# Performance work log

Hardware: AMD Instinct MI355X
Metric: run time of the kernel (lower is better)

## Reference

```python
import jax, jax.numpy as jnp
import numpy as np

K = 2            # top-k experts
SCALING = 16.0 / 16.0  # alpha / r


def setup_inputs() -> dict:
    key = jax.random.key(0)
    ks = jax.random.split(key, 7)
    B, T, D, O, E, R = 2, 4096, 2048, 2048, 8, 16
    return {
        "x": jax.random.normal(ks[0], (B, T, D), dtype=jnp.float32),
        "W": jax.random.normal(ks[1], (O, D), dtype=jnp.float32) * (1.0 / np.sqrt(D)),
        "b": jax.random.normal(ks[2], (O,), dtype=jnp.float32) * 0.02,
        "lora_A": jax.random.normal(ks[3], (E, R, D), dtype=jnp.float32) * (1.0 / np.sqrt(D)),
        "lora_B": jax.random.normal(ks[4], (E, O, R), dtype=jnp.float32) * 0.02,
        "gate_w": jax.random.normal(ks[5], (E, D), dtype=jnp.float32) * 0.02,
        "gate_b": jax.random.normal(ks[6], (E,), dtype=jnp.float32) * 0.02,
    }


def reference(x, W, b, lora_A, lora_B, gate_w, gate_b):
    orig_shape = x.shape
    D = orig_shape[-1]
    O = W.shape[0]
    x_flat = x.reshape(-1, D)                                  # [N, D]

    base = x_flat @ W.T + b                                    # [N, O]

    logits = x_flat @ gate_w.T + gate_b                        # [N, E] (eval: no noise)
    topk_logits, topk_idx = jax.lax.top_k(logits, K)           # [N, K]
    gates = jax.nn.softmax(topk_logits, axis=-1)               # [N, K]

    xA = jnp.einsum('nd,erd->ner', x_flat, lora_A)             # [N, E, R]
    delta_all = jnp.einsum('ner,eor->neo', xA, lora_B)         # [N, E, O]

    delta_topk = jnp.take_along_axis(delta_all, topk_idx[:, :, None], axis=1)  # [N, K, O]
    lora_update = jnp.sum(delta_topk * gates[:, :, None], axis=1)              # [N, O]

    out = base + SCALING * lora_update
    return out.reshape(*orig_shape[:-1], O)
```

## Files before the change

### kernel.cpp

```cpp
#include <hip/hip_runtime.h>
#include <hip/hip_bf16.h>
#include <stdint.h>

#define N_ROWS 8192
#define DIM    2048
#define OUTD   2048
#define NEXP   8
#define RNK    16
#define ZCOLS  128
#define KAUG   2176

typedef unsigned short u16;
typedef float  f32x4  __attribute__((ext_vector_type(4)));
typedef __bf16 bf16x8 __attribute__((ext_vector_type(8)));

__device__ __forceinline__ u16 f2bf(float f) {
  unsigned u = __float_as_uint(f);
  return (u16)((u + 0x7fffu + ((u >> 16) & 1u)) >> 16);
}

__global__ __launch_bounds__(256) void k1_convert_gate(
    const float* __restrict__ x, const float* __restrict__ gw,
    const float* __restrict__ gb, u16* __restrict__ xaug,
    int* __restrict__ sel, float* __restrict__ gv)
{
  const int wave = threadIdx.x >> 6;
  const int lane = threadIdx.x & 63;
  const int row0 = blockIdx.x * 8 + wave * 2;

  float xv[2][32];
  #pragma unroll
  for (int rr = 0; rr < 2; ++rr) {
    const float* xr = x + (size_t)(row0 + rr) * DIM;
    #pragma unroll
    for (int i = 0; i < 8; ++i) {
      float4 v = *(const float4*)(xr + (lane * 4 + i * 256));
      xv[rr][i*4+0] = v.x; xv[rr][i*4+1] = v.y;
      xv[rr][i*4+2] = v.z; xv[rr][i*4+3] = v.w;
    }
  }
  #pragma unroll
  for (int rr = 0; rr < 2; ++rr) {
    u16* dst = xaug + (size_t)(row0 + rr) * KAUG;
    #pragma unroll
    for (int i = 0; i < 8; ++i) {
      ushort4 s;
      s.x = f2bf(xv[rr][i*4+0]); s.y = f2bf(xv[rr][i*4+1]);
      s.z = f2bf(xv[rr][i*4+2]); s.w = f2bf(xv[rr][i*4+3]);
      *(ushort4*)(dst + (lane * 4 + i * 256)) = s;
    }
  }
  float lg[2][NEXP];
  #pragma unroll
  for (int e = 0; e < NEXP; ++e) {
    const float* ge = gw + (size_t)e * DIM;
    float s0 = 0.f, s1 = 0.f;
    #pragma unroll
    for (int i = 0; i < 8; ++i) {
      float4 g4 = *(const float4*)(ge + (lane * 4 + i * 256));
      s0 += xv[0][i*4+0]*g4.x + xv[0][i*4+1]*g4.y + xv[0][i*4+2]*g4.z + xv[0][i*4+3]*g4.w;
      s1 += xv[1][i*4+0]*g4.x + xv[1][i*4+1]*g4.y + xv[1][i*4+2]*g4.z + xv[1][i*4+3]*g4.w;
    }
    #pragma unroll
    for (int off = 32; off > 0; off >>= 1) {
      s0 += __shfl_xor(s0, off);
      s1 += __shfl_xor(s1, off);
    }
    lg[0][e] = s0 + gb[e];
    lg[1][e] = s1 + gb[e];
  }
  if (lane == 0) {
    #pragma unroll
    for (int rr = 0; rr < 2; ++rr) {
      int e0 = 0; float m0 = lg[rr][0];
      #pragma unroll
      for (int e = 1; e < NEXP; ++e) if (lg[rr][e] > m0) { m0 = lg[rr][e]; e0 = e; }
      int e1 = (e0 == 0) ? 1 : 0; float m1 = lg[rr][e1];
      #pragma unroll
      for (int e = 0; e < NEXP; ++e) if (e != e0 && lg[rr][e] > m1) { m1 = lg[rr][e]; e1 = e; }
      float t   = expf(m1 - m0);
      float inv = 1.f / (1.f + t);
      int r = row0 + rr;
      sel[2*r] = e0; sel[2*r+1] = e1;
      gv[2*r]  = inv; gv[2*r+1] = t * inv;
    }
  }
}

__global__ __launch_bounds__(256) void k2_weights(
    const float* __restrict__ W, const float* __restrict__ lB,
    const float* __restrict__ lA, u16* __restrict__ waug, u16* __restrict__ ab)
{
  const int t = threadIdx.x;
  const int bid = blockIdx.x;
  if (bid < OUTD) {
    const int o = bid;
    const float* wr = W + (size_t)o * DIM;
    u16* dst = waug + (size_t)o * KAUG;
    #pragma unroll
    for (int i = 0; i < 2; ++i) {
      int c = t * 4 + i * 1024;
      float4 v = *(const float4*)(wr + c);
      ushort4 s; s.x = f2bf(v.x); s.y = f2bf(v.y); s.z = f2bf(v.z); s.w = f2bf(v.w);
      *(ushort4*)(dst + c) = s;
    }
    if (t < ZCOLS) {
      int e = t >> 4, r = t & 15;
      dst[DIM + t] = f2bf(lB[((size_t)e * OUTD + o) * RNK + r]);
    }
  } else {
    const int ar = bid - OUTD;
    const float* src = lA + (size_t)ar * DIM;
    u16* dst = ab + (size_t)ar * DIM;
    #pragma unroll
    for (int i = 0; i < 2; ++i) {
      int c = t * 4 + i * 1024;
      float4 v = *(const float4*)(src + c);
      ushort4 s; s.x = f2bf(v.x); s.y = f2bf(v.y); s.z = f2bf(v.z); s.w = f2bf(v.w);
      *(ushort4*)(dst + c) = s;
    }
  }
}

template <int BM, int BN, int BK, int WM, int WN, int MF, int NF, int EPI>
__global__ __launch_bounds__(WM*WN*64) void gemm_bt(
    const u16* __restrict__ A, int lda,
    const u16* __restrict__ Bm, int ldb,
    int Ksz, int grid_n,
    float* __restrict__ outF, int ldo, const float* __restrict__ bias,
    u16* __restrict__ outZ, int ldz,
    const int* __restrict__ sel, const float* __restrict__ gv)
{
  static_assert(BM == WM * MF * 16 && BN == WN * NF * 16 && BK == 64, "geom");
  constexpr int NW   = WM * WN;
  constexpr int ROWB = BK * 2;
  __shared__ __align__(16) u16 As[2][BM * BK];
  __shared__ __align__(16) u16 Bs[2][BN * BK];

  const int wave = threadIdx.x >> 6;
  const int lane = threadIdx.x & 63;

  int bid = blockIdx.x;
  const int nwg = gridDim.x;
  if ((nwg & 7) == 0) {
    const int cpx = nwg >> 3;
    bid = (bid & 7) * cpx + (bid >> 3);
  }
  const int tm = bid / grid_n;
  const int tn = bid % grid_n;
  const size_t row0 = (size_t)tm * BM;
  const size_t col0 = (size_t)tn * BN;

  auto stage = [&](const u16* __restrict__ g, int ld, size_t r0, int k0,
                   u16* lds, int nrows) {
    const int nch = nrows * (ROWB / 16);
    for (int c0 = wave * 64; c0 < nch; c0 += NW * 64) {
      const int c   = c0 + lane;
      const int r   = c >> 3;
      const int ch  = c & 7;
      const int sch = ch ^ (r & 7);
      const char* src = (const char*)(g + (r0 + (size_t)r) * ld + k0) + (sch << 4);
      __builtin_amdgcn_global_load_lds(
          (__attribute__((address_space(1))) void*)src,
          (__attribute__((address_space(3))) void*)((char*)lds + ((size_t)c0 << 4)),
          16, 0, 0);
    }
  };

  const int wm = wave / WN, wn = wave % WN;
  const int aRow = wm * MF * 16 + (lane & 15);
  const int bRow = wn * NF * 16 + (lane & 15);
  const int kq   = (lane >> 4) << 4;

  f32x4 acc[MF][NF] = {};

  const int nk = Ksz / BK;
  stage(A,  lda, row0, 0, As[0], BM);
  stage(Bm, ldb, col0, 0, Bs[0], BN);
  __syncthreads();

  for (int t = 0; t < nk; ++t) {
    const int cur = t & 1;
    if (t + 1 < nk) {
      stage(A,  lda, row0, (t + 1) * BK, As[cur ^ 1], BM);
      stage(Bm, ldb, col0, (t + 1) * BK, Bs[cur ^ 1], BN);
    }
    const char* ab_ = (const char*)As[cur];
    const char* bb_ = (const char*)Bs[cur];
    #pragma unroll
    for (int ks = 0; ks < BK / 32; ++ks) {
      bf16x8 av[MF], bv[NF];
      #pragma unroll
      for (int mf = 0; mf < MF; ++mf) {
        const int r  = aRow + mf * 16;
        const int bo = (ks * 64 + kq) ^ ((r & 7) << 4);
        av[mf] = *(const bf16x8*)(ab_ + r * ROWB + bo);
      }
      #pragma unroll
      for (int nf = 0; nf < NF; ++nf) {
        const int r  = bRow + nf * 16;
        const int bo = (ks * 64 + kq) ^ ((r & 7) << 4);
        bv[nf] = *(const bf16x8*)(bb_ + r * ROWB + bo);
      }
      #pragma unroll
      for (int mf = 0; mf < MF; ++mf)
        #pragma unroll
        for (int nf = 0; nf < NF; ++nf)
          acc[mf][nf] = __builtin_amdgcn_mfma_f32_16x16x32_bf16(
              av[mf], bv[nf], acc[mf][nf], 0, 0, 0);
    }
    __syncthreads();
  }

  if constexpr (EPI == 1) {
    #pragma unroll
    for (int nf = 0; nf < NF; ++nf) {
      const size_t c = col0 + wn * NF * 16 + nf * 16 + (lane & 15);
      const float bvv = bias[c];
      #pragma unroll
      for (int mf = 0; mf < MF; ++mf) {
        const size_t rb = row0 + wm * MF * 16 + mf * 16 + ((lane >> 4) << 2);
        #pragma unroll
        for (int j = 0; j < 4; ++j)
          outF[(rb + j) * (size_t)ldo + c] = acc[mf][nf][j] + bvv;
      }
    }
  } else {
    #pragma unroll
    for (int mf = 0; mf < MF; ++mf) {
      const size_t rb = row0 + wm * MF * 16 + mf * 16 + ((lane >> 4) << 2);
      #pragma unroll
      for (int j = 0; j < 4; ++j) {
        const size_t rrow = rb + j;
        const int   e0 = sel[2 * rrow],     e1 = sel[2 * rrow + 1];
        const float g0 = gv [2 * rrow],     g1 = gv [2 * rrow + 1];
        #pragma unroll
        for (int nf = 0; nf < NF; ++nf) {
          const int ccol = wn * NF * 16 + nf * 16 + (lane & 15);
          const int e = ccol >> 4;
          const float s = (e == e0) ? g0 : ((e == e1) ? g1 : 0.f);
          outZ[rrow * (size_t)ldz + ccol] = f2bf(acc[mf][nf][j] * s);
        }
      }
    }
  }
}

__global__ __launch_bounds__(512, 2) void gemm256_pipe(
    const u16* __restrict__ A, int lda,
    const u16* __restrict__ Bm, int ldb,
    int Ksz, int grid_n,
    float* __restrict__ outF, int ldo, const float* __restrict__ bias)
{
  __shared__ __align__(16) u16 smem[65536];

  const int tid  = threadIdx.x;
  const int wave = tid >> 6;
  const int lane = tid & 63;

  int bid = blockIdx.x;
  const int nwg = gridDim.x;
  if ((nwg & 7) == 0) {
    const int cpx = nwg >> 3;
    bid = (bid & 7) * cpx + (bid >> 3);
  }
  const int tm = bid / grid_n;
  const int tn = bid % grid_n;
  const size_t row0 = (size_t)tm * 256;
  const size_t col0 = (size_t)tn * 256;

  const int rc  = tid >> 2;
  const int sch = (tid & 3) ^ (rc & 3);
  const char* aS0 = (const char*)(A  + (row0 + (size_t)rc)         * lda) + (sch << 4);
  const char* aS1 = (const char*)(A  + (row0 + (size_t)(rc + 128)) * lda) + (sch << 4);
  const char* bS0 = (const char*)(Bm + (col0 + (size_t)rc)         * ldb) + (sch << 4);
  const char* bS1 = (const char*)(Bm + (col0 + (size_t)(rc + 128)) * ldb) + (sch << 4);
  char* ldsA = (char*)smem + wave * 1024;
  char* ldsB = (char*)smem + 65536 + wave * 1024;

  auto stage = [&](int tt) {
    const size_t ko = (size_t)tt << 6;
    const int    sb = (tt & 3) << 14;
    __builtin_amdgcn_global_load_lds(
        (__attribute__((address_space(1))) void*)(aS0 + ko),
        (__attribute__((address_space(3))) void*)(ldsA + sb), 16, 0, 0);
    __builtin_amdgcn_global_load_lds(
        (__attribute__((address_space(1))) void*)(aS1 + ko),
        (__attribute__((address_space(3))) void*)(ldsA + sb + 8192), 16, 0, 0);
    __builtin_amdgcn_global_load_lds(
        (__attribute__((address_space(1))) void*)(bS0 + ko),
        (__attribute__((address_space(3))) void*)(ldsB + sb), 16, 0, 0);
    __builtin_amdgcn_global_load_lds(
        (__attribute__((address_space(1))) void*)(bS1 + ko),
        (__attribute__((address_space(3))) void*)(ldsB + sb + 8192), 16, 0, 0);
  };

  const int wm = wave >> 2, wn = wave & 3;
  const int swzk = ((lane >> 4) ^ (lane & 3)) << 4;
  const int offA = (wm * 128 + (lane & 15)) * 64 + swzk;
  const int offB = (wn * 64  + (lane & 15)) * 64 + swzk;

  f32x4 acc[8][4] = {};

  const int nk = Ksz / 32;
  stage(0); stage(1); stage(2);

  for (int t = 0; t < nk; ++t) {
    if      (t + 2 < nk) asm volatile("s_waitcnt vmcnt(8)" ::: "memory");
    else if (t + 1 < nk) asm volatile("s_waitcnt vmcnt(4)" ::: "memory");
    else                 asm volatile("s_waitcnt vmcnt(0)" ::: "memory");
    __builtin_amdgcn_s_barrier();
    __builtin_amdgcn_sched_barrier(0);

    if (t + 3 < nk) stage(t + 3);

    const char* sa = (const char*)smem + ((t & 3) << 14);
    const char* sb = (const char*)smem + 65536 + ((t & 3) << 14);

    bf16x8 av[8], bv[4];
    #pragma unroll
    for (int mf = 0; mf < 8; ++mf)
      av[mf] = *(const bf16x8*)(sa + offA + mf * 1024);
    #pragma unroll
    for (int nf = 0; nf < 4; ++nf)
      bv[nf] = *(const bf16x8*)(sb + offB + nf * 1024);

    __builtin_amdgcn_s_setprio(1);
    #pragma unroll
    for (int mf = 0; mf < 8; ++mf)
      #pragma unroll
      for (int nf = 0; nf < 4; ++nf)
        acc[mf][nf] = __builtin_amdgcn_mfma_f32_16x16x32_bf16(
            av[mf], bv[nf], acc[mf][nf], 0, 0, 0);
    __builtin_amdgcn_s_setprio(0);
  }

  #pragma unroll
  for (int nf = 0; nf < 4; ++nf) {
    const size_t c = col0 + wn * 64 + nf * 16 + (lane & 15);
    const float bvv = bias[c];
    #pragma unroll
    for (int mf = 0; mf < 8; ++mf) {
      const size_t rb = row0 + wm * 128 + mf * 16 + ((lane >> 4) << 2);
      #pragma unroll
      for (int j = 0; j < 4; ++j)
        outF[(rb + j) * (size_t)ldo + c] = acc[mf][nf][j] + bvv;
    }
  }
}

extern "C" void kernel_launch(void* const* d_in, const int* in_sizes, int n_in,
                              void* d_out, int out_size, void* d_ws, size_t ws_size,
                              hipStream_t stream) {
  const float* x  = (const float*)d_in[0];
  const float* W  = (const float*)d_in[1];
  const float* b  = (const float*)d_in[2];
  const float* lA = (const float*)d_in[3];
  const float* lB = (const float*)d_in[4];
  const float* gw = (const float*)d_in[5];
  const float* gb = (const float*)d_in[6];
  float* out = (float*)d_out;

  u16*   xaug = (u16*)d_ws;
  u16*   waug = xaug + (size_t)N_ROWS * KAUG;
  u16*   ab   = waug + (size_t)OUTD * KAUG;
  int*   sel  = (int*)(ab + (size_t)ZCOLS * DIM);
  float* gv   = (float*)(sel + 2 * N_ROWS);

  hipLaunchKernelGGL(k1_convert_gate, dim3(N_ROWS / 8), dim3(256), 0, stream,
                     x, gw, gb, xaug, sel, gv);
  hipLaunchKernelGGL(k2_weights, dim3(OUTD + ZCOLS), dim3(256), 0, stream,
                     W, lB, lA, waug, ab);
  hipLaunchKernelGGL((gemm_bt<32, 128, 64, 1, 4, 2, 2, 0>),
                     dim3(N_ROWS / 32), dim3(256), 0, stream,
                     xaug, KAUG, ab, DIM, DIM, 1,
                     (float*)nullptr, 0, (const float*)nullptr,
                     xaug + DIM, KAUG, sel, gv);
  hipLaunchKernelGGL(gemm256_pipe,
                     dim3((N_ROWS / 256) * (OUTD / 256)), dim3(512), 0, stream,
                     xaug, KAUG, waug, KAUG, KAUG, OUTD / 256,
                     out, OUTD, b);
}
```

Baseline: 141.7 us.

## Split-K the LoRA-A GEMM with a separate reduce-gate kernel and use BK=64 main pipeline

The x·A^T GEMM is now a split-K kernel with 128x128 tiles over four K slices. It writes fp32 partials that a new kernel sums, scales by the top-k gate and packs as bf16 into the augmented activation columns. The goal is more parallelism and better tile reuse for the narrow 128-column GEMM. The main 256x256 GEMM moves from a 4-stage BK=32 pipeline to a 2-stage BK=64 one, with two MFMA sub-steps and an extra barrier before the next stage is issued. The cost is an extra kernel launch, fp32 partial traffic through workspace, and less prefetch depth in the main GEMM.

```diff
diff --git a/kernel.cpp b/kernel.cpp
--- a/kernel.cpp
+++ b/kernel.cpp
@@ -9,6 +9,8 @@
 #define RNK    16
 #define ZCOLS  128
 #define KAUG   2176
+#define KSPLIT 4
+#define KSLICE (DIM / KSPLIT)
 
 typedef unsigned short u16;
 typedef float  f32x4  __attribute__((ext_vector_type(4)));
@@ -122,14 +124,11 @@
   }
 }
 
-template <int BM, int BN, int BK, int WM, int WN, int MF, int NF, int EPI>
-__global__ __launch_bounds__(WM*WN*64) void gemm_bt(
+template <int BM, int BN, int BK, int WM, int WN, int MF, int NF>
+__global__ __launch_bounds__(WM*WN*64) void gemm_ksplit(
     const u16* __restrict__ A, int lda,
     const u16* __restrict__ Bm, int ldb,
-    int Ksz, int grid_n,
-    float* __restrict__ outF, int ldo, const float* __restrict__ bias,
-    u16* __restrict__ outZ, int ldz,
-    const int* __restrict__ sel, const float* __restrict__ gv)
+    int Ksz, int gm, float* __restrict__ outP)
 {
   static_assert(BM == WM * MF * 16 && BN == WN * NF * 16 && BK == 64, "geom");
   constexpr int NW   = WM * WN;
@@ -146,10 +145,11 @@
     const int cpx = nwg >> 3;
     bid = (bid & 7) * cpx + (bid >> 3);
   }
-  const int tm = bid / grid_n;
-  const int tn = bid % grid_n;
+  const int tm  = bid % gm;
+  const int ksl = bid / gm;
   const size_t row0 = (size_t)tm * BM;
-  const size_t col0 = (size_t)tn * BN;
+  const u16* Ak = A  + (size_t)ksl * Ksz;
+  const u16* Bk = Bm + (size_t)ksl * Ksz;
 
   auto stage = [&](const u16* __restrict__ g, int ld, size_t r0, int k0,
                    u16* lds, int nrows) {
@@ -175,15 +175,15 @@
   f32x4 acc[MF][NF] = {};
 
   const int nk = Ksz / BK;
-  stage(A,  lda, row0, 0, As[0], BM);
-  stage(Bm, ldb, col0, 0, Bs[0], BN);
+  stage(Ak, lda, row0, 0, As[0], BM);
+  stage(Bk, ldb, 0,    0, Bs[0], BN);
   __syncthreads();
 
   for (int t = 0; t < nk; ++t) {
     const int cur = t & 1;
     if (t + 1 < nk) {
-      stage(A,  lda, row0, (t + 1) * BK, As[cur ^ 1], BM);
-      stage(Bm, ldb, col0, (t + 1) * BK, Bs[cur ^ 1], BN);
+      stage(Ak, lda, row0, (t + 1) * BK, As[cur ^ 1], BM);
+      stage(Bk, ldb, 0,    (t + 1) * BK, Bs[cur ^ 1], BN);
     }
     const char* ab_ = (const char*)As[cur];
     const char* bb_ = (const char*)Bs[cur];
@@ -212,38 +212,42 @@
     __syncthreads();
   }
 
-  if constexpr (EPI == 1) {
-    #pragma unroll
-    for (int nf = 0; nf < NF; ++nf) {
-      const size_t c = col0 + wn * NF * 16 + nf * 16 + (lane & 15);
-      const float bvv = bias[c];
-      #pragma unroll
-      for (int mf = 0; mf < MF; ++mf) {
-        const size_t rb = row0 + wm * MF * 16 + mf * 16 + ((lane >> 4) << 2);
-        #pragma unroll
-        for (int j = 0; j < 4; ++j)
-          outF[(rb + j) * (size_t)ldo + c] = acc[mf][nf][j] + bvv;
-      }
-    }
-  } else {
+  float* op = outP + (size_t)ksl * N_ROWS * ZCOLS;
+  #pragma unroll
+  for (int nf = 0; nf < NF; ++nf) {
+    const int c = wn * NF * 16 + nf * 16 + (lane & 15);
     #pragma unroll
     for (int mf = 0; mf < MF; ++mf) {
       const size_t rb = row0 + wm * MF * 16 + mf * 16 + ((lane >> 4) << 2);
       #pragma unroll
-      for (int j = 0; j < 4; ++j) {
-        const size_t rrow = rb + j;
-        const int   e0 = sel[2 * rrow],     e1 = sel[2 * rrow + 1];
-        const float g0 = gv [2 * rrow],     g1 = gv [2 * rrow + 1];
-        #pragma unroll
-        for (int nf = 0; nf < NF; ++nf) {
-          const int ccol = wn * NF * 16 + nf * 16 + (lane & 15);
-          const int e = ccol >> 4;
-          const float s = (e == e0) ? g0 : ((e == e1) ? g1 : 0.f);
-          outZ[rrow * (size_t)ldz + ccol] = f2bf(acc[mf][nf][j] * s);
-        }
-      }
-    }
-  }
+      for (int j = 0; j < 4; ++j)
+        op[(rb + j) * ZCOLS + c] = acc[mf][nf][j];
+    }
+  }
+}
+
+__global__ __launch_bounds__(256) void k3b_reduce_gate(
+    const float* __restrict__ zpart, const int* __restrict__ sel,
+    const float* __restrict__ gv, u16* __restrict__ xaug)
+{
+  const int idx = blockIdx.x * 256 + threadIdx.x;
+  const int row = idx >> 5;
+  const int c4  = (idx & 31) << 2;
+  const float* zr = zpart + (size_t)row * ZCOLS + c4;
+  const size_t sl = (size_t)N_ROWS * ZCOLS;
+  float4 s = *(const float4*)zr;
+  #pragma unroll
+  for (int k = 1; k < KSPLIT; ++k) {
+    float4 v = *(const float4*)(zr + k * sl);
+    s.x += v.x; s.y += v.y; s.z += v.z; s.w += v.w;
+  }
+  const int e  = c4 >> 4;
+  const int e0 = sel[2 * row], e1 = sel[2 * row + 1];
+  const float g = (e == e0) ? gv[2 * row] : ((e == e1) ? gv[2 * row + 1] : 0.f);
+  ushort4 o;
+  o.x = f2bf(s.x * g); o.y = f2bf(s.y * g);
+  o.z = f2bf(s.z * g); o.w = f2bf(s.w * g);
+  *(ushort4*)(xaug + (size_t)row * KAUG + DIM + c4) = o;
 }
 
 __global__ __launch_bounds__(512, 2) void gemm256_pipe(
@@ -269,62 +273,71 @@
   const size_t row0 = (size_t)tm * 256;
   const size_t col0 = (size_t)tn * 256;
 
-  const int rc  = tid >> 2;
-  const int sch = (tid & 3) ^ (rc & 3);
-  const char* aS0 = (const char*)(A  + (row0 + (size_t)rc)         * lda) + (sch << 4);
-  const char* aS1 = (const char*)(A  + (row0 + (size_t)(rc + 128)) * lda) + (sch << 4);
-  const char* bS0 = (const char*)(Bm + (col0 + (size_t)rc)         * ldb) + (sch << 4);
-  const char* bS1 = (const char*)(Bm + (col0 + (size_t)(rc + 128)) * ldb) + (sch << 4);
+  const int l3  = lane >> 3;
+  const int sch = ((lane & 7) ^ l3) << 4;
+  const char* aSrc = (const char*)(A  + (row0 + (size_t)(wave * 8 + l3)) * lda) + sch;
+  const char* bSrc = (const char*)(Bm + (col0 + (size_t)(wave * 8 + l3)) * ldb) + sch;
+  const size_t arst = (size_t)lda * 128;
+  const size_t brst = (size_t)ldb * 128;
   char* ldsA = (char*)smem + wave * 1024;
   char* ldsB = (char*)smem + 65536 + wave * 1024;
 
   auto stage = [&](int tt) {
-    const size_t ko = (size_t)tt << 6;
-    const int    sb = (tt & 3) << 14;
-    __builtin_amdgcn_global_load_lds(
-        (__attribute__((address_space(1))) void*)(aS0 + ko),
-        (__attribute__((address_space(3))) void*)(ldsA + sb), 16, 0, 0);
-    __builtin_amdgcn_global_load_lds(
-        (__attribute__((address_space(1))) void*)(aS1 + ko),
-        (__attribute__((address_space(3))) void*)(ldsA + sb + 8192), 16, 0, 0);
-    __builtin_amdgcn_global_load_lds(
-        (__attribute__((address_space(1))) void*)(bS0 + ko),
-        (__attribute__((address_space(3))) void*)(ldsB + sb), 16, 0, 0);
-    __builtin_amdgcn_global_load_lds(
-        (__attribute__((address_space(1))) void*)(bS1 + ko),
-        (__attribute__((address_space(3))) void*)(ldsB + sb + 8192), 16, 0, 0);
+    const size_t ko = (size_t)tt * 128;
+    const int    sb = (tt & 1) << 15;
+    #pragma unroll
+    for (int i = 0; i < 4; ++i)
+      __builtin_amdgcn_global_load_lds(
+          (__attribute__((address_space(1))) void*)(aSrc + ko + i * arst),
+          (__attribute__((address_space(3))) void*)(ldsA + sb + i * 8192), 16, 0, 0);
+    #pragma unroll
+    for (int i = 0; i < 4; ++i)
+      __builtin_amdgcn_global_load_lds(
+          (__attribute__((address_space(1))) void*)(bSrc + ko + i * brst),
+          (__attribute__((address_space(3))) void*)(ldsB + sb + i * 8192), 16, 0, 0);
   };
 
   const int wm = wave >> 2, wn = wave & 3;
-  const int swzk = ((lane >> 4) ^ (lane & 3)) << 4;
-  const int offA = (wm * 128 + (lane & 15)) * 64 + swzk;
-  const int offB = (wn * 64  + (lane & 15)) * 64 + swzk;
+  const int x0 = ((lane >> 4) ^ (lane & 7)) << 4;
+  const int offA0 = wm * 16384 + (lane & 15) * 128 + x0;
+  const int offB0 = wn * 8192  + (lane & 15) * 128 + x0;
 
   f32x4 acc[8][4] = {};
 
-  const int nk = Ksz / 32;
-  stage(0); stage(1); stage(2);
+  const int nk = Ksz / 64;
+  stage(0); stage(1);
 
   for (int t = 0; t < nk; ++t) {
-    if      (t + 2 < nk) asm volatile("s_waitcnt vmcnt(8)" ::: "memory");
-    else if (t + 1 < nk) asm volatile("s_waitcnt vmcnt(4)" ::: "memory");
-    else                 asm volatile("s_waitcnt vmcnt(0)" ::: "memory");
+    if (t + 1 < nk) asm volatile("s_waitcnt vmcnt(8)" ::: "memory");
+    else            asm volatile("s_waitcnt vmcnt(0)" ::: "memory");
     __builtin_amdgcn_s_barrier();
     __builtin_amdgcn_sched_barrier(0);
 
-    if (t + 3 < nk) stage(t + 3);
-
-    const char* sa = (const char*)smem + ((t & 3) << 14);
-    const char* sb = (const char*)smem + 65536 + ((t & 3) << 14);
+    const char* sa = (const char*)smem + ((t & 1) << 15);
+    const char* sb = (const char*)smem + 65536 + ((t & 1) << 15);
 
     bf16x8 av[8], bv[4];
     #pragma unroll
+    for (int mf = 0; mf < 8; ++mf) av[mf] = *(const bf16x8*)(sa + offA0 + mf * 2048);
+    #pragma unroll
+    for (int nf = 0; nf < 4; ++nf) bv[nf] = *(const bf16x8*)(sb + offB0 + nf * 2048);
+    __builtin_amdgcn_s_setprio(1);
+    #pragma unroll
     for (int mf = 0; mf < 8; ++mf)
-      av[mf] = *(const bf16x8*)(sa + offA + mf * 1024);
-    #pragma unroll
-    for (int nf = 0; nf < 4; ++nf)
-      bv[nf] = *(const bf16x8*)(sb + offB + nf * 1024);
-
+      #pragma unroll
+      for (int nf = 0; nf < 4; ++nf)
+        acc[mf][nf] = __builtin_amdgcn_mfma_f32_16x16x32_bf16(
+            av[mf], bv[nf], acc[mf][nf], 0, 0, 0);
+    __builtin_amdgcn_s_setprio(0);
+
+    #pragma unroll
+    for (int mf = 0; mf < 8; ++mf) av[mf] = *(const bf16x8*)(sa + (offA0 ^ 64) + mf * 2048);
+    #pragma unroll
+    for (int nf = 0; nf < 4; ++nf) bv[nf] = *(const bf16x8*)(sb + (offB0 ^ 64) + nf * 2048);
+    asm volatile("s_waitcnt lgkmcnt(0)" ::: "memory");
+    __builtin_amdgcn_s_barrier();
+    __builtin_amdgcn_sched_barrier(0);
+    if (t + 2 < nk) stage(t + 2);
     __builtin_amdgcn_s_setprio(1);
     #pragma unroll
     for (int mf = 0; mf < 8; ++mf)
@@ -361,21 +374,22 @@
   const float* gb = (const float*)d_in[6];
   float* out = (float*)d_out;
 
-  u16*   xaug = (u16*)d_ws;
-  u16*   waug = xaug + (size_t)N_ROWS * KAUG;
-  u16*   ab   = waug + (size_t)OUTD * KAUG;
-  int*   sel  = (int*)(ab + (size_t)ZCOLS * DIM);
-  float* gv   = (float*)(sel + 2 * N_ROWS);
+  u16*   xaug  = (u16*)d_ws;
+  u16*   waug  = xaug + (size_t)N_ROWS * KAUG;
+  u16*   ab    = waug + (size_t)OUTD * KAUG;
+  int*   sel   = (int*)(ab + (size_t)ZCOLS * DIM);
+  float* gv    = (float*)(sel + 2 * N_ROWS);
+  float* zpart = (float*)(gv + 2 * N_ROWS);
 
   hipLaunchKernelGGL(k1_convert_gate, dim3(N_ROWS / 8), dim3(256), 0, stream,
                      x, gw, gb, xaug, sel, gv);
   hipLaunchKernelGGL(k2_weights, dim3(OUTD + ZCOLS), dim3(256), 0, stream,
                      W, lB, lA, waug, ab);
-  hipLaunchKernelGGL((gemm_bt<32, 128, 64, 1, 4, 2, 2, 0>),
-                     dim3(N_ROWS / 32), dim3(256), 0, stream,
-                     xaug, KAUG, ab, DIM, DIM, 1,
-                     (float*)nullptr, 0, (const float*)nullptr,
-                     xaug + DIM, KAUG, sel, gv);
+  hipLaunchKernelGGL((gemm_ksplit<128, 128, 64, 2, 2, 4, 4>),
+                     dim3((N_ROWS / 128) * KSPLIT), dim3(256), 0, stream,
+                     xaug, KAUG, ab, DIM, KSLICE, N_ROWS / 128, zpart);
+  hipLaunchKernelGGL(k3b_reduce_gate, dim3(N_ROWS * 32 / 256), dim3(256), 0, stream,
+                     zpart, sel, gv, xaug);
   hipLaunchKernelGGL(gemm256_pipe,
                      dim3((N_ROWS / 256) * (OUTD / 256)), dim3(512), 0, stream,
                      xaug, KAUG, waug, KAUG, KAUG, OUTD / 256,
```

Measured after the change: 126.3 us. 1.12x faster.
